# Kernel tuning notes

Hardware: AMD Instinct MI355X
Metric: run time of the kernel (lower is better)

## Reference

```python
import jax, jax.numpy as jnp
import numpy as np

N_NODES = 100000
N_EDGES = 3200000
F_IN = 256
HEADS = 8
C_OUT = 8
NEG_SLOPE = 0.2


def setup_inputs() -> dict:
    key = jax.random.key(0)
    k1, k2, k3, k4, k5, k6 = jax.random.split(key, 6)
    x = jax.random.normal(k1, (N_NODES, F_IN), dtype=jnp.float32)
    edge_index = jax.random.randint(k2, (2, N_EDGES), 0, N_NODES, dtype=jnp.int64)
    W = jax.random.normal(k3, (F_IN, HEADS * C_OUT), dtype=jnp.float32) * (1.0 / np.sqrt(F_IN))
    att_src = jax.random.normal(k4, (HEADS, C_OUT), dtype=jnp.float32) * 0.1
    att_dst = jax.random.normal(k5, (HEADS, C_OUT), dtype=jnp.float32) * 0.1
    bias = jax.random.normal(k6, (HEADS * C_OUT,), dtype=jnp.float32) * 0.01
    return {"x": x, "edge_index": edge_index, "W": W, "att_src": att_src, "att_dst": att_dst, "bias": bias}


def reference(x, edge_index, W, att_src, att_dst, bias):
    # GATConv (PyG semantics), concat=True, inference (dropout off).
    N = x.shape[0]
    H, C = att_src.shape
    h = (x @ W).reshape(N, H, C)                      # [N,H,C] transformed features
    a_src = jnp.einsum('nhc,hc->nh', h, att_src)      # [N,H]
    a_dst = jnp.einsum('nhc,hc->nh', h, att_dst)      # [N,H]
    src, dst = edge_index[0], edge_index[1]
    # per-edge raw attention logits
    e = jax.nn.leaky_relu(a_src[src] + a_dst[dst], NEG_SLOPE)  # [E,H]
    # segment softmax over incoming edges of each destination node
    m = jax.ops.segment_max(e, dst, num_segments=N)            # [N,H]
    e = jnp.exp(e - m[dst])
    s = jax.ops.segment_sum(e, dst, num_segments=N)            # [N,H]
    alpha = e / (s[dst] + 1e-16)                               # [E,H]
    # scatter-add weighted neighbor features
    out = jax.ops.segment_sum(alpha[:, :, None] * h[src], dst, num_segments=N)  # [N,H,C]
    return out.reshape(N, H * C) + bias
```

## Files before the change

### kernel.cpp

```cpp
#include <hip/hip_runtime.h>
#include <hip/hip_fp16.h>
#include <math.h>

#define F_IN 256
#define HC 64
#define NHEAD 8
#define NEG 0.2f
#define BSH 7
#define BSZ 128
#define CAP 5376

typedef __attribute__((ext_vector_type(8))) short bf16x8;
typedef __attribute__((ext_vector_type(4))) float f32x4;

union BV { uint4 q; bf16x8 v; };

__device__ __forceinline__ unsigned int hi_pair(float a, float b) {
  return (__float_as_uint(b) & 0xffff0000u) | (__float_as_uint(a) >> 16);
}
__device__ __forceinline__ unsigned int lo_pair(float a, float b) {
  float ra = a - __uint_as_float(__float_as_uint(a) & 0xffff0000u);
  float rb = b - __uint_as_float(__float_as_uint(b) & 0xffff0000u);
  return (__float_as_uint(rb) & 0xffff0000u) | (__float_as_uint(ra) >> 16);
}

__global__ __launch_bounds__(256) void k_prep(const float* __restrict__ W,
                                              unsigned short* __restrict__ Wp,
                                              int* __restrict__ bcursor, int NB) {
  int b = blockIdx.x, t = threadIdx.x;
  if (b >= 64) {
    int i = (b - 64) * 256 + t;
    if (i < NB) bcursor[i] = 0;
    return;
  }
  int idx = b * 256 + t;
  int k = idx >> 6, c = idx & 63;
  float w = W[idx];
  unsigned int u = __float_as_uint(w);
  unsigned short hi = (unsigned short)((u + 0x7fffu + ((u >> 16) & 1u)) >> 16);
  float r = w - __uint_as_float((unsigned int)hi << 16);
  unsigned int ur = __float_as_uint(r);
  unsigned short lo = (unsigned short)((ur + 0x7fffu + ((ur >> 16) & 1u)) >> 16);
  int ks = k >> 5, j = k & 7, lg = (k >> 3) & 3;
  int lane = lg * 16 + (c & 15), cg = c >> 4;
  int off = ((ks * 4 + cg) * 64 + lane) * 8 + j;
  Wp[off] = hi;
  Wp[16384 + off] = lo;
}

__global__ __launch_bounds__(256, 3) void k_gemm(
    const float* __restrict__ x, const uint4* __restrict__ Wp4,
    const float* __restrict__ att_src, const float* __restrict__ att_dst,
    __half2* __restrict__ h2, float* __restrict__ asrc, float* __restrict__ adst, int N) {
  int t = threadIdx.x;
  int wv = t >> 6, l = t & 63;
  int lr = l & 15, lg = l >> 4;
  int r0 = blockIdx.x * 128 + wv * 32;
  int ra = r0 + lr;      if (ra > N - 1) ra = N - 1;
  int rb = r0 + 16 + lr; if (rb > N - 1) rb = N - 1;
  const float* xr0 = x + (size_t)ra * F_IN + lg * 8;
  const float* xr1 = x + (size_t)rb * F_IN + lg * 8;
  const uint4* wp = Wp4 + l;

  float as4[4], ad4[4];
#pragma unroll
  for (int cg = 0; cg < 4; cg++) {
    as4[cg] = att_src[cg * 16 + lr];
    ad4[cg] = att_dst[cg * 16 + lr];
  }

  f32x4 acc[2][4];
#pragma unroll
  for (int i = 0; i < 2; i++)
#pragma unroll
    for (int j = 0; j < 4; j++) acc[i][j] = (f32x4){0.f, 0.f, 0.f, 0.f};

#pragma unroll
  for (int ks = 0; ks < 8; ks++) {
    float4 p0 = *(const float4*)(xr0 + ks * 32);
    float4 q0 = *(const float4*)(xr0 + ks * 32 + 4);
    float4 p1 = *(const float4*)(xr1 + ks * 32);
    float4 q1 = *(const float4*)(xr1 + ks * 32 + 4);
    BV bh[4], bl[4];
#pragma unroll
    for (int cg = 0; cg < 4; cg++) {
      bh[cg].q = wp[(ks * 4 + cg) * 64];
      bl[cg].q = wp[2048 + (ks * 4 + cg) * 64];
    }
    BV ah0, al0, ah1, al1;
    ah0.q.x = hi_pair(p0.x, p0.y); ah0.q.y = hi_pair(p0.z, p0.w);
    ah0.q.z = hi_pair(q0.x, q0.y); ah0.q.w = hi_pair(q0.z, q0.w);
    al0.q.x = lo_pair(p0.x, p0.y); al0.q.y = lo_pair(p0.z, p0.w);
    al0.q.z = lo_pair(q0.x, q0.y); al0.q.w = lo_pair(q0.z, q0.w);
    ah1.q.x = hi_pair(p1.x, p1.y); ah1.q.y = hi_pair(p1.z, p1.w);
    ah1.q.z = hi_pair(q1.x, q1.y); ah1.q.w = hi_pair(q1.z, q1.w);
    al1.q.x = lo_pair(p1.x, p1.y); al1.q.y = lo_pair(p1.z, p1.w);
    al1.q.z = lo_pair(q1.x, q1.y); al1.q.w = lo_pair(q1.z, q1.w);
#pragma unroll
    for (int cg = 0; cg < 4; cg++) {
      acc[0][cg] = __builtin_amdgcn_mfma_f32_16x16x32_bf16(ah0.v, bh[cg].v, acc[0][cg], 0, 0, 0);
      acc[0][cg] = __builtin_amdgcn_mfma_f32_16x16x32_bf16(al0.v, bh[cg].v, acc[0][cg], 0, 0, 0);
      acc[0][cg] = __builtin_amdgcn_mfma_f32_16x16x32_bf16(ah0.v, bl[cg].v, acc[0][cg], 0, 0, 0);
      acc[1][cg] = __builtin_amdgcn_mfma_f32_16x16x32_bf16(ah1.v, bh[cg].v, acc[1][cg], 0, 0, 0);
      acc[1][cg] = __builtin_amdgcn_mfma_f32_16x16x32_bf16(al1.v, bh[cg].v, acc[1][cg], 0, 0, 0);
      acc[1][cg] = __builtin_amdgcn_mfma_f32_16x16x32_bf16(ah1.v, bl[cg].v, acc[1][cg], 0, 0, 0);
    }
  }

#pragma unroll
  for (int rg = 0; rg < 2; rg++) {
#pragma unroll
    for (int tt = 0; tt < 4; tt++) {
      int node = r0 + rg * 16 + 4 * lg + tt;
      bool ok = node < N;
      float v0 = acc[rg][0][tt], v1 = acc[rg][1][tt], v2 = acc[rg][2][tt], v3 = acc[rg][3][tt];
      float o0 = __shfl_xor(v0, 1), o1 = __shfl_xor(v1, 1);
      float o2 = __shfl_xor(v2, 1), o3 = __shfl_xor(v3, 1);
      if (ok && !(l & 1)) {
        size_t hb = (size_t)node * 32 + (lr >> 1);
        h2[hb]      = __halves2half2(__float2half_rn(v0), __float2half_rn(o0));
        h2[hb + 8]  = __halves2half2(__float2half_rn(v1), __float2half_rn(o1));
        h2[hb + 16] = __halves2half2(__float2half_rn(v2), __float2half_rn(o2));
        h2[hb + 24] = __halves2half2(__float2half_rn(v3), __float2half_rn(o3));
      }
#pragma unroll
      for (int cg = 0; cg < 4; cg++) {
        float v = (cg == 0) ? v0 : (cg == 1) ? v1 : (cg == 2) ? v2 : v3;
        float s = v * as4[cg];
        float d = v * ad4[cg];
        s += __shfl_xor(s, 1); d += __shfl_xor(d, 1);
        s += __shfl_xor(s, 2); d += __shfl_xor(d, 2);
        s += __shfl_xor(s, 4); d += __shfl_xor(d, 4);
        if (ok && !(l & 7)) {
          int hd = 2 * cg + (lr >> 3);
          asrc[node * NHEAD + hd] = s;
          adst[node * NHEAD + hd] = d;
        }
      }
    }
  }
}

__global__ __launch_bounds__(512) void k_partition(
    const int* __restrict__ edge, int* __restrict__ bcursor,
    unsigned int* __restrict__ entries, int E, int NB) {
  __shared__ unsigned long long srt8[8192];
  __shared__ int hist[1024];
  __shared__ int loff[1024];
  __shared__ int basearr[1024];
  __shared__ int pr[512];
  int t = threadIdx.x;
  int base = blockIdx.x * 8192;
  int cblk = min(8192, E - base);
  for (int i = t; i < 1024; i += 512) hist[i] = 0;
  __syncthreads();
#pragma unroll
  for (int j = 0; j < 16; j++) {
    int e = base + j * 512 + t;
    if (e < E) atomicAdd(&hist[edge[E + e] >> BSH], 1);
  }
  __syncthreads();
  int a = hist[2 * t], b = hist[2 * t + 1];
  pr[t] = a + b;
  __syncthreads();
  for (int off = 1; off < 512; off <<= 1) {
    int add = (t >= off) ? pr[t - off] : 0;
    __syncthreads();
    pr[t] += add;
    __syncthreads();
  }
  int excl = pr[t] - (a + b);
  loff[2 * t] = excl;
  loff[2 * t + 1] = excl + a;
  if (a > 0 && 2 * t < NB) basearr[2 * t] = atomicAdd(&bcursor[2 * t], a);
  if (b > 0 && 2 * t + 1 < NB) basearr[2 * t + 1] = atomicAdd(&bcursor[2 * t + 1], b);
  hist[2 * t] = excl;
  hist[2 * t + 1] = excl + a;
  __syncthreads();
#pragma unroll
  for (int j = 0; j < 16; j++) {
    int e = base + j * 512 + t;
    if (e < E) {
      int s = edge[e], d = edge[E + e];
      int p = atomicAdd(&hist[d >> BSH], 1);
      srt8[p] = ((unsigned long long)(unsigned int)d << 32) | (unsigned int)s;
    }
  }
  __syncthreads();
  for (int i = t; i < cblk; i += 512) {
    unsigned long long v = srt8[i];
    int d = (int)(v >> 32), s = (int)(v & 0xFFFFFFFFu);
    int bk = d >> BSH;
    int local = basearr[bk] + (i - loff[bk]);
    if (local < CAP)
      entries[(size_t)bk * CAP + local] = ((unsigned int)(d & (BSZ - 1)) << 17) | (unsigned int)s;
  }
}

__global__ __launch_bounds__(512, 6) void k_bagg(
    const unsigned int* __restrict__ entries, const int* __restrict__ bcursor,
    const __half2* __restrict__ h2, const float* __restrict__ asrc,
    const float* __restrict__ adst, const float* __restrict__ bias,
    float* __restrict__ out, int N) {
  __shared__ int srt[CAP];
  __shared__ int hist[BSZ];
  __shared__ int cur[BSZ];
  __shared__ int off[BSZ + 1];
  __shared__ int tmp[BSZ];
  int t = threadIdx.x;
  int bkt = blockIdx.x;
  int n0 = bkt << BSH;
  int ncnt = min(BSZ, N - n0);
  int cnt = bcursor[bkt];
  if (cnt > CAP) cnt = CAP;
  const unsigned int* ebase = entries + (size_t)bkt * CAP;
  for (int i = t; i < BSZ; i += 512) hist[i] = 0;
  __syncthreads();
  for (int i = t; i < cnt; i += 512)
    atomicAdd(&hist[ebase[i] >> 17], 1);
  __syncthreads();
  if (t < BSZ) tmp[t] = hist[t];
  __syncthreads();
  for (int o = 1; o < BSZ; o <<= 1) {
    int add = (t < BSZ && t >= o) ? tmp[t - o] : 0;
    __syncthreads();
    if (t < BSZ) tmp[t] += add;
    __syncthreads();
  }
  if (t < BSZ) { off[t] = tmp[t] - hist[t]; cur[t] = tmp[t] - hist[t]; }
  if (t == 0) off[BSZ] = cnt;
  __syncthreads();
  for (int i = t; i < cnt; i += 512) {
    unsigned int v = ebase[i];
    int p = atomicAdd(&cur[v >> 17], 1);
    srt[p] = (int)(v & 0x1FFFF);
  }
  __syncthreads();
  int wv = t >> 6, lane = t & 63;
  int sub = lane >> 5, sl = lane & 31;
  int head = sl >> 2;
  for (int nd = wv; nd < ncnt; nd += 8) {
    int node = n0 + nd;
    int sbeg = off[nd], send = off[nd + 1];
    float ad = adst[node * NHEAD + head];
    float ax = 0.f, ay = 0.f, wsum = 0.f;
    int k = sbeg + sub;
    for (; k + 6 < send; k += 8) {
      int s0 = srt[k];
      int s1 = srt[k + 2];
      int s2 = srt[k + 4];
      int s3 = srt[k + 6];
      float l0 = asrc[s0 * NHEAD + head] + ad;
      float l1 = asrc[s1 * NHEAD + head] + ad;
      float l2 = asrc[s2 * NHEAD + head] + ad;
      float l3 = asrc[s3 * NHEAD + head] + ad;
      __half2 v0 = h2[(size_t)s0 * 32 + sl];
      __half2 v1 = h2[(size_t)s1 * 32 + sl];
      __half2 v2 = h2[(size_t)s2 * 32 + sl];
      __half2 v3 = h2[(size_t)s3 * 32 + sl];
      float w0 = __expf(fmaxf(l0, NEG * l0));
      float w1 = __expf(fmaxf(l1, NEG * l1));
      float w2 = __expf(fmaxf(l2, NEG * l2));
      float w3 = __expf(fmaxf(l3, NEG * l3));
      float2 f0 = __half22float2(v0);
      float2 f1 = __half22float2(v1);
      float2 f2 = __half22float2(v2);
      float2 f3 = __half22float2(v3);
      ax = fmaf(w0, f0.x, fmaf(w1, f1.x, fmaf(w2, f2.x, fmaf(w3, f3.x, ax))));
      ay = fmaf(w0, f0.y, fmaf(w1, f1.y, fmaf(w2, f2.y, fmaf(w3, f3.y, ay))));
      wsum += (w0 + w1) + (w2 + w3);
    }
    for (; k < send; k += 2) {
      int s = srt[k];
      float lg = asrc[s * NHEAD + head] + ad;
      float w = __expf(fmaxf(lg, NEG * lg));
      float2 f = __half22float2(h2[(size_t)s * 32 + sl]);
      ax = fmaf(w, f.x, ax);
      ay = fmaf(w, f.y, ay);
      wsum += w;
    }
    ax += __shfl_xor(ax, 32);
    ay += __shfl_xor(ay, 32);
    wsum += __shfl_xor(wsum, 32);
    if (sub == 0) {
      float inv = wsum > 0.f ? 1.0f / wsum : 0.f;
      float2 bx = *(const float2*)&bias[2 * sl];
      float2 r;
      r.x = fmaf(ax, inv, bx.x);
      r.y = fmaf(ay, inv, bx.y);
      *(float2*)&out[(size_t)node * HC + 2 * sl] = r;
    }
  }
}

extern "C" void kernel_launch(void* const* d_in, const int* in_sizes, int n_in,
                              void* d_out, int out_size, void* d_ws, size_t ws_size,
                              hipStream_t stream) {
  const float* x = (const float*)d_in[0];
  const int* edge = (const int*)d_in[1];
  const float* W = (const float*)d_in[2];
  const float* att_src = (const float*)d_in[3];
  const float* att_dst = (const float*)d_in[4];
  const float* bias = (const float*)d_in[5];
  int N = in_sizes[0] / F_IN;
  int E = in_sizes[1] / 2;
  float* out = (float*)d_out;
  int NB = (N + BSZ - 1) >> BSH;

  unsigned short* Wp = (unsigned short*)d_ws;
  __half2* h2 = (__half2*)((char*)d_ws + 65536);
  float* asrc = (float*)(h2 + (size_t)N * 32);
  float* adst = asrc + (size_t)N * NHEAD;
  int* bcursor = (int*)(adst + (size_t)N * NHEAD);
  unsigned int* entries = (unsigned int*)(bcursor + ((NB + 3) & ~3));

  int nch = (E + 8191) / 8192;
  int nzb = (NB + 255) / 256;

  k_prep<<<64 + nzb, 256, 0, stream>>>(W, Wp, bcursor, NB);
  k_gemm<<<(N + 127) / 128, 256, 0, stream>>>(x, (const uint4*)Wp, att_src, att_dst, h2, asrc, adst, N);
  k_partition<<<nch, 512, 0, stream>>>(edge, bcursor, entries, E, NB);
  k_bagg<<<NB, 512, 0, stream>>>(entries, bcursor, h2, asrc, adst, bias, out, N);
}
```

Measured before the change: 330.4 us.

## Remap aggregation lanes to 8 edges by 8 heads with 16-byte gathers

Changes the per-node aggregation thread mapping. Before, two half-waves each took alternating edges and every lane loaded one half2 channel pair. Now the wave processes 8 edges at once, each lane loads a full head (8 halfs) with one uint4 load and keeps 8 accumulators. A butterfly shuffle reduction across edge slots follows. This cuts per-edge index and asrc loads and widens memory transactions, but adds masking of idle slots for low-degree nodes, an 8-register accumulator set, and a longer 3-step shuffle reduction over 9 values.

```diff
diff --git a/kernel.cpp b/kernel.cpp
--- a/kernel.cpp
+++ b/kernel.cpp
@@ -236,59 +236,53 @@
     srt[p] = (int)(v & 0x1FFFF);
   }
   __syncthreads();
-  int wv = t >> 6, lane = t & 63;
-  int sub = lane >> 5, sl = lane & 31;
-  int head = sl >> 2;
+  int wv = t >> 6, l = t & 63;
+  int eslot = l >> 3, cg = l & 7;
   for (int nd = wv; nd < ncnt; nd += 8) {
     int node = n0 + nd;
     int sbeg = off[nd], send = off[nd + 1];
-    float ad = adst[node * NHEAD + head];
-    float ax = 0.f, ay = 0.f, wsum = 0.f;
-    int k = sbeg + sub;
-    for (; k + 6 < send; k += 8) {
-      int s0 = srt[k];
-      int s1 = srt[k + 2];
-      int s2 = srt[k + 4];
-      int s3 = srt[k + 6];
-      float l0 = asrc[s0 * NHEAD + head] + ad;
-      float l1 = asrc[s1 * NHEAD + head] + ad;
-      float l2 = asrc[s2 * NHEAD + head] + ad;
-      float l3 = asrc[s3 * NHEAD + head] + ad;
-      __half2 v0 = h2[(size_t)s0 * 32 + sl];
-      __half2 v1 = h2[(size_t)s1 * 32 + sl];
-      __half2 v2 = h2[(size_t)s2 * 32 + sl];
-      __half2 v3 = h2[(size_t)s3 * 32 + sl];
-      float w0 = __expf(fmaxf(l0, NEG * l0));
-      float w1 = __expf(fmaxf(l1, NEG * l1));
-      float w2 = __expf(fmaxf(l2, NEG * l2));
-      float w3 = __expf(fmaxf(l3, NEG * l3));
-      float2 f0 = __half22float2(v0);
-      float2 f1 = __half22float2(v1);
-      float2 f2 = __half22float2(v2);
-      float2 f3 = __half22float2(v3);
-      ax = fmaf(w0, f0.x, fmaf(w1, f1.x, fmaf(w2, f2.x, fmaf(w3, f3.x, ax))));
-      ay = fmaf(w0, f0.y, fmaf(w1, f1.y, fmaf(w2, f2.y, fmaf(w3, f3.y, ay))));
-      wsum += (w0 + w1) + (w2 + w3);
-    }
-    for (; k < send; k += 2) {
-      int s = srt[k];
-      float lg = asrc[s * NHEAD + head] + ad;
+    float ad = adst[node * NHEAD + cg];
+    float a0 = 0.f, a1 = 0.f, a2 = 0.f, a3 = 0.f;
+    float a4 = 0.f, a5 = 0.f, a6 = 0.f, a7 = 0.f;
+    float wsum = 0.f;
+    for (int k = sbeg; k < send; k += 8) {
+      int idx = k + eslot;
+      bool val = idx < send;
+      int s = srt[val ? idx : send - 1];
+      float lg = asrc[s * NHEAD + cg] + ad;
       float w = __expf(fmaxf(lg, NEG * lg));
-      float2 f = __half22float2(h2[(size_t)s * 32 + sl]);
-      ax = fmaf(w, f.x, ax);
-      ay = fmaf(w, f.y, ay);
+      w = val ? w : 0.f;
+      union { uint4 q; __half2 h[4]; } u;
+      u.q = *((const uint4*)(h2 + (size_t)s * 32) + cg);
+      float2 f0 = __half22float2(u.h[0]);
+      float2 f1 = __half22float2(u.h[1]);
+      float2 f2 = __half22float2(u.h[2]);
+      float2 f3 = __half22float2(u.h[3]);
+      a0 = fmaf(w, f0.x, a0); a1 = fmaf(w, f0.y, a1);
+      a2 = fmaf(w, f1.x, a2); a3 = fmaf(w, f1.y, a3);
+      a4 = fmaf(w, f2.x, a4); a5 = fmaf(w, f2.y, a5);
+      a6 = fmaf(w, f3.x, a6); a7 = fmaf(w, f3.y, a7);
       wsum += w;
     }
-    ax += __shfl_xor(ax, 32);
-    ay += __shfl_xor(ay, 32);
-    wsum += __shfl_xor(wsum, 32);
-    if (sub == 0) {
+#pragma unroll
+    for (int m = 8; m < 64; m <<= 1) {
+      a0 += __shfl_xor(a0, m); a1 += __shfl_xor(a1, m);
+      a2 += __shfl_xor(a2, m); a3 += __shfl_xor(a3, m);
+      a4 += __shfl_xor(a4, m); a5 += __shfl_xor(a5, m);
+      a6 += __shfl_xor(a6, m); a7 += __shfl_xor(a7, m);
+      wsum += __shfl_xor(wsum, m);
+    }
+    if (l < 8) {
       float inv = wsum > 0.f ? 1.0f / wsum : 0.f;
-      float2 bx = *(const float2*)&bias[2 * sl];
-      float2 r;
-      r.x = fmaf(ax, inv, bx.x);
-      r.y = fmaf(ay, inv, bx.y);
-      *(float2*)&out[(size_t)node * HC + 2 * sl] = r;
+      float4 b0 = *(const float4*)&bias[cg * 8];
+      float4 b1 = *(const float4*)&bias[cg * 8 + 4];
+      float4 r0, r1;
+      r0.x = fmaf(a0, inv, b0.x); r0.y = fmaf(a1, inv, b0.y);
+      r0.z = fmaf(a2, inv, b0.z); r0.w = fmaf(a3, inv, b0.w);
+      r1.x = fmaf(a4, inv, b1.x); r1.y = fmaf(a5, inv, b1.y);
+      r1.z = fmaf(a6, inv, b1.z); r1.w = fmaf(a7, inv, b1.w);
+      *(float4*)&out[(size_t)node * HC + cg * 8] = r0;
+      *(float4*)&out[(size_t)node * HC + cg * 8 + 4] = r1;
     }
   }
 }
```

New measurement: 325.8 us. About the same (-1.4%).
